# Kernel optimization log

Hardware: AMD Instinct MI355X
Metric: run time of the kernel (lower is better)

Reference implementation:

```python
import jax, jax.numpy as jnp
import numpy as np

L, D, H, FF = 4, 256, 8, 1024
B, S = 4, 1024
HD = D // H
EPS = 1e-5


def layer_norm(x, g, b):
    mu = jnp.mean(x, axis=-1, keepdims=True)
    var = jnp.mean(jnp.square(x - mu), axis=-1, keepdims=True)
    return (x - mu) * jax.lax.rsqrt(var + EPS) * g + b


def setup_inputs() -> dict:
    key = jax.random.key(0)
    ks = jax.random.split(key, 16)
    sd = 0.02
    return {
        "x": jax.random.normal(ks[0], (B, S, D), dtype=jnp.float32),
        "mask": jnp.ones((B, S), dtype=jnp.int32),
        # per-layer stacked params (leading dim L); Linear stored as (in, out)
        "qkv_w": jax.random.normal(ks[1], (L, D, 3 * D), dtype=jnp.float32) * sd,
        "qkv_b": jnp.zeros((L, 3 * D), dtype=jnp.float32),
        "fc_w": jax.random.normal(ks[2], (L, D, D), dtype=jnp.float32) * sd,
        "fc_b": jnp.zeros((L, D), dtype=jnp.float32),
        "ln1_g": jnp.ones((L, D), dtype=jnp.float32),
        "ln1_b": jnp.zeros((L, D), dtype=jnp.float32),
        "ln2_g": jnp.ones((L, D), dtype=jnp.float32),
        "ln2_b": jnp.zeros((L, D), dtype=jnp.float32),
        "ff1_w": jax.random.normal(ks[3], (L, D, FF), dtype=jnp.float32) * sd,
        "ff1_b": jnp.zeros((L, FF), dtype=jnp.float32),
        "ff2_w": jax.random.normal(ks[4], (L, FF, D), dtype=jnp.float32) * sd,
        "ff2_b": jnp.zeros((L, D), dtype=jnp.float32),
    }


def reference(x, mask, qkv_w, qkv_b, fc_w, fc_b, ln1_g, ln1_b, ln2_g, ln2_b,
              ff1_w, ff1_b, ff2_w, ff2_b):
    # mask: 1 = valid token, 0 = pad
    neg_inf = jnp.finfo(x.dtype).min
    key_mask = (mask == 0)[:, None, None, :]  # [B,1,1,S]
    for l in range(L):
        residual = x
        qkv = x @ qkv_w[l] + qkv_b[l]                       # [B,S,3D]
        q, k, v = jnp.split(qkv, 3, axis=-1)
        q = q.reshape(B, S, H, HD).transpose(0, 2, 1, 3)    # [B,H,S,hd]
        k = k.reshape(B, S, H, HD).transpose(0, 2, 1, 3)
        v = v.reshape(B, S, H, HD).transpose(0, 2, 1, 3)
        attn = jnp.einsum('bhqd,bhkd->bhqk', q, k)          # scale=1 (scale=False)
        attn = jnp.where(key_mask, neg_inf, attn)
        attn = jax.nn.softmax(attn, axis=-1)
        o = jnp.einsum('bhqk,bhkd->bhqd', attn, v)
        o = o.transpose(0, 2, 1, 3).reshape(B, S, D)
        o = o @ fc_w[l] + fc_b[l]
        x = layer_norm(o + residual, ln1_g[l], ln1_b[l])    # after_norm=True
        residual = x
        h = jax.nn.relu(x @ ff1_w[l] + ff1_b[l])
        h = h @ ff2_w[l] + ff2_b[l]
        x = layer_norm(residual + h, ln2_g[l], ln2_b[l])
    return x
```

## Files before the change

### kernel.cpp

```cpp
#include <hip/hip_runtime.h>
#include <hip/hip_bf16.h>
#include <math.h>

#define NL 4
#define DMODEL 256
#define NH 8
#define FFDIM 1024
#define BB 4
#define SS 1024
#define HDIM 32
#define MROWS (BB * SS)
#define LN_EPS 1e-5f

typedef __bf16 bf16x8 __attribute__((ext_vector_type(8)));
typedef float f32x4 __attribute__((ext_vector_type(4)));
typedef short s16x4 __attribute__((ext_vector_type(4)));
typedef unsigned int u32;

__device__ __forceinline__ ushort f2bf(float f) {
    uint u = __builtin_bit_cast(uint, f);
    u += 0x7fff + ((u >> 16) & 1);
    return (ushort)(u >> 16);
}
__device__ __forceinline__ uint pack2(float a, float b) {
    return (uint)f2bf(a) | ((uint)f2bf(b) << 16);
}

__device__ __forceinline__ int xcd_swz(int bid, int nwg) {
    return (bid & 7) * (nwg >> 3) + (bid >> 3);
}

template<int N> __device__ __forceinline__ void vmcnt_wait() {
    asm volatile("s_waitcnt vmcnt(%0)" :: "n"(N) : "memory");
}
__device__ __forceinline__ void raw_barrier() {
    asm volatile("s_barrier" ::: "memory");
}
__device__ __forceinline__ void lgkm0() {
    asm volatile("s_waitcnt lgkmcnt(0)" ::: "memory");
}

__device__ __forceinline__ void async_ld16(const void* g, void* l) {
    __builtin_amdgcn_global_load_lds(
        (const __attribute__((address_space(1))) u32*)g,
        (__attribute__((address_space(3))) u32*)l, 16, 0, 0);
}

#if __has_builtin(__builtin_amdgcn_ds_read_tr16_b64)
#define TR_BUILTIN 1
#else
#define TR_BUILTIN 0
#endif

__device__ __forceinline__ s16x4 tr16(const ushort* p) {
    __attribute__((address_space(3))) s16x4* ap =
        (__attribute__((address_space(3))) s16x4*)p;
#if TR_BUILTIN
    return __builtin_amdgcn_ds_read_tr16_b64(ap);
#else
    s16x4 r;
    asm volatile("ds_read_b64_tr_b16 %0, %1" : "=v"(r) : "v"(ap) : "memory");
    return r;
#endif
}
__device__ __forceinline__ void tr_fence() {
#if !TR_BUILTIN
    asm volatile("s_waitcnt lgkmcnt(0)" ::: "memory");
    __builtin_amdgcn_sched_barrier(0);
#endif
}

__global__ __launch_bounds__(256)
void wconv_all(const float* __restrict__ qkv_w, const float* __restrict__ fc_w,
               const float* __restrict__ ff1_w, const float* __restrict__ ff2_w,
               ushort* __restrict__ wq, ushort* __restrict__ wfc,
               ushort* __restrict__ wf1, ushort* __restrict__ wf2)
{
    const int l = blockIdx.z;
    int t = blockIdx.x;
    const float* src; ushort* dst; int K, N, nx;
    if (t < 192)      {          src = qkv_w; dst = wq;  K = 256;  N = 768;  nx = 24; }
    else if (t < 256) { t -= 192; src = fc_w;  dst = wfc; K = 256;  N = 256;  nx = 8; }
    else if (t < 512) { t -= 256; src = ff1_w; dst = wf1; K = 256;  N = 1024; nx = 32; }
    else              { t -= 512; src = ff2_w; dst = wf2; K = 1024; N = 256;  nx = 8; }
    src += (size_t)l * K * N;
    dst += (size_t)l * K * N;
    const int n0 = (t % nx) * 32, k0 = (t / nx) * 32;

    __shared__ ushort tt[32][33];
    const int tn = threadIdx.x & 31, tk8 = threadIdx.x >> 5;
    #pragma unroll
    for (int i = 0; i < 4; ++i)
        tt[tn][tk8 + i * 8] = f2bf(src[(size_t)(k0 + tk8 + i * 8) * N + n0 + tn]);
    __syncthreads();
    #pragma unroll
    for (int i = 0; i < 4; ++i)
        dst[(size_t)(n0 + tk8 + i * 8) * K + k0 + tn] = tt[tk8 + i * 8][tn];
}

__global__ __launch_bounds__(256)
void convert_x(const float* __restrict__ xin, float* __restrict__ x,
               ushort* __restrict__ xb)
{
    const size_t i = ((size_t)blockIdx.x * 256 + threadIdx.x) * 4;
    const float4 v = *reinterpret_cast<const float4*>(xin + i);
    *reinterpret_cast<float4*>(x + i) = v;
    uint2 p = make_uint2(pack2(v.x, v.y), pack2(v.z, v.w));
    *reinterpret_cast<uint2*>(xb + i) = p;
}

template<int BM, int BN, int WM, int WN, int ACT, int OBF>
__global__ __launch_bounds__(256)
void gemm_mfma(const ushort* __restrict__ A, const ushort* __restrict__ WT,
               const float* __restrict__ bias, float* __restrict__ Cf,
               ushort* __restrict__ Cb, int N, int K)
{
    constexpr int BK = 64;
    constexpr int WR = BM / WM;
    constexpr int WC = BN / WN;
    constexpr int MR = WR / 16, NR = WC / 16;
    constexpr int LSTG = BM / 32 + BN / 32;
    __shared__ __align__(16) ushort As[2][BM * BK];
    __shared__ __align__(16) ushort Bs[2][BN * BK];

    const int tid = threadIdx.x;
    const int lin = blockIdx.y * gridDim.x + blockIdx.x;
    const int work = xcd_swz(lin, gridDim.x * gridDim.y);
    const int m0 = (work / gridDim.x) * BM, n0 = (work % gridDim.x) * BN;
    const int wid = tid >> 6, lane = tid & 63;
    const int g = lane >> 4, c = lane & 15;
    const int wr = wid / WN, wc = wid % WN;

    auto stage = [&](int buf, int k0) {
        #pragma unroll
        for (int it = 0; it < (BM * BK * 2) / 4096; ++it) {
            const int o = tid * 16 + it * 4096;
            const int r = o >> 7;
            const int cb = (o & 127) ^ ((r & 7) << 4);
            async_ld16(A + (size_t)(m0 + r) * K + k0 + (cb >> 1),
                       (char*)&As[buf][0] + o);
        }
        #pragma unroll
        for (int it = 0; it < (BN * BK * 2) / 4096; ++it) {
            const int o = tid * 16 + it * 4096;
            const int r = o >> 7;
            const int cb = (o & 127) ^ ((r & 7) << 4);
            async_ld16(WT + (size_t)(n0 + r) * K + k0 + (cb >> 1),
                       (char*)&Bs[buf][0] + o);
        }
    };

    f32x4 acc[MR][NR] = {};

    stage(0, 0);

    int cur = 0;
    for (int k0 = 0; k0 < K; k0 += BK, cur ^= 1) {
        if (k0 + BK < K) { stage(cur ^ 1, k0 + BK); vmcnt_wait<LSTG>(); }
        else             { vmcnt_wait<0>(); }
        raw_barrier();

        #pragma unroll
        for (int ks = 0; ks < 2; ++ks) {
            bf16x8 af[MR], bfr[NR];
            #pragma unroll
            for (int mi = 0; mi < MR; ++mi) {
                const int row = wr * WR + mi * 16 + c;
                af[mi] = *(const bf16x8*)((const char*)&As[cur][0]
                    + row * 128 + ((ks * 64 + g * 16) ^ ((row & 7) << 4)));
            }
            #pragma unroll
            for (int ni = 0; ni < NR; ++ni) {
                const int row = wc * WC + ni * 16 + c;
                bfr[ni] = *(const bf16x8*)((const char*)&Bs[cur][0]
                    + row * 128 + ((ks * 64 + g * 16) ^ ((row & 7) << 4)));
            }
            #pragma unroll
            for (int mi = 0; mi < MR; ++mi)
                #pragma unroll
                for (int ni = 0; ni < NR; ++ni)
                    acc[mi][ni] = __builtin_amdgcn_mfma_f32_16x16x32_bf16(
                        af[mi], bfr[ni], acc[mi][ni], 0, 0, 0);
        }
        raw_barrier();
    }

    float bv[NR];
    #pragma unroll
    for (int ni = 0; ni < NR; ++ni)
        bv[ni] = bias[n0 + wc * WC + ni * 16 + c];

    #pragma unroll
    for (int mi = 0; mi < MR; ++mi) {
        #pragma unroll
        for (int j = 0; j < 4; ++j) {
            const int row = m0 + wr * WR + mi * 16 + g * 4 + j;
            #pragma unroll
            for (int ni = 0; ni < NR; ++ni) {
                float v = acc[mi][ni][j] + bv[ni];
                if (ACT) v = fmaxf(v, 0.f);
                const int col = n0 + wc * WC + ni * 16 + c;
                if (OBF) Cb[(size_t)row * N + col] = f2bf(v);
                else     Cf[(size_t)row * N + col] = v;
            }
        }
    }
}

__global__ __launch_bounds__(256)
void mlp_fused(const ushort* __restrict__ Aattn, const ushort* __restrict__ Wfc,
               const float* __restrict__ bfc, const float* __restrict__ g1,
               const float* __restrict__ be1, const ushort* __restrict__ W1,
               const float* __restrict__ b1, const ushort* __restrict__ W2,
               const float* __restrict__ b2, const float* __restrict__ g2,
               const float* __restrict__ be2, float* __restrict__ x,
               ushort* __restrict__ xb)
{
    __shared__ __align__(16) ushort As[2][16 * 64];
    __shared__ __align__(16) ushort Bs[2][256 * 64];
    __shared__ __align__(16) ushort ybf[16 * 256];
    __shared__ __align__(16) ushort hbuf[16 * 1024];
    __shared__ float rsum[4][16], rsq[4][16], mval[16], ival[16];

    const int tid = threadIdx.x;
    const int m0 = blockIdx.x * 16;
    const int wid = tid >> 6, lane = tid & 63;
    const int g = lane >> 4, c = lane & 15;

    auto stageB = [&](int buf, const ushort* src, int ldk) {
        #pragma unroll
        for (int it = 0; it < 8; ++it) {
            const int o = tid * 16 + it * 4096;
            const int r = o >> 7;
            const int cb = (o & 127) ^ ((r & 7) << 4);
            async_ld16(src + (size_t)r * ldk + (cb >> 1), (char*)&Bs[buf][0] + o);
        }
    };
    auto stageA = [&](int buf, int k0) {
        if (tid < 128) {
            const int o = tid * 16;
            const int r = o >> 7;
            const int cb = (o & 127) ^ ((r & 7) << 4);
            async_ld16(Aattn + (size_t)(m0 + r) * 256 + k0 + (cb >> 1),
                       (char*)&As[buf][0] + o);
        }
    };

    f32x4 acc[4] = {};
    const f32x4 zf = {0.f, 0.f, 0.f, 0.f};

    stageA(0, 0); stageB(0, Wfc, 256);
    int cur = 0;
    #pragma unroll
    for (int k = 0; k < 4; ++k, cur ^= 1) {
        if (k < 3) {
            stageA(cur ^ 1, (k + 1) * 64);
            stageB(cur ^ 1, Wfc + (k + 1) * 64, 256);
            if (tid < 128) vmcnt_wait<9>(); else vmcnt_wait<8>();
        } else {
            stageB(cur ^ 1, W1, 256);
            vmcnt_wait<8>();
        }
        raw_barrier();
        #pragma unroll
        for (int ks = 0; ks < 2; ++ks) {
            const bf16x8 af = *(const bf16x8*)((const char*)&As[cur][0]
                + c * 128 + ((ks * 64 + g * 16) ^ ((c & 7) << 4)));
            #pragma unroll
            for (int ni = 0; ni < 4; ++ni) {
                const int row = wid * 64 + ni * 16 + c;
                const bf16x8 bf = *(const bf16x8*)((const char*)&Bs[cur][0]
                    + row * 128 + ((ks * 64 + g * 16) ^ ((row & 7) << 4)));
                acc[ni] = __builtin_amdgcn_mfma_f32_16x16x32_bf16(af, bf, acc[ni], 0, 0, 0);
            }
        }
        raw_barrier();
    }

    float res[4][4];
    {
        float bv[4], gl[4], bl[4];
        #pragma unroll
        for (int ni = 0; ni < 4; ++ni) {
            const int col = wid * 64 + ni * 16 + c;
            bv[ni] = bfc[col]; gl[ni] = g1[col]; bl[ni] = be1[col];
        }
        #pragma unroll
        for (int j = 0; j < 4; ++j) {
            const int row = g * 4 + j;
            float s = 0.f;
            #pragma unroll
            for (int ni = 0; ni < 4; ++ni) {
                const int col = wid * 64 + ni * 16 + c;
                float vv = acc[ni][j] + bv[ni] + x[(size_t)(m0 + row) * 256 + col];
                acc[ni][j] = vv;
                s += vv;
            }
            #pragma unroll
            for (int off = 1; off < 16; off <<= 1) s += __shfl_xor(s, off);
            if (c == 0) rsum[wid][row] = s;
        }
        __syncthreads();
        if (tid < 16)
            mval[tid] = (rsum[0][tid] + rsum[1][tid] + rsum[2][tid] + rsum[3][tid])
                        * (1.f / 256);
        __syncthreads();
        #pragma unroll
        for (int j = 0; j < 4; ++j) {
            const int row = g * 4 + j;
            const float mean = mval[row];
            float q = 0.f;
            #pragma unroll
            for (int ni = 0; ni < 4; ++ni) {
                const float d = acc[ni][j] - mean;
                q += d * d;
            }
            #pragma unroll
            for (int off = 1; off < 16; off <<= 1) q += __shfl_xor(q, off);
            if (c == 0) rsq[wid][row] = q;
        }
        __syncthreads();
        if (tid < 16) {
            const float q = rsq[0][tid] + rsq[1][tid] + rsq[2][tid] + rsq[3][tid];
            ival[tid] = rsqrtf(q * (1.f / 256) + LN_EPS);
        }
        __syncthreads();
        #pragma unroll
        for (int j = 0; j < 4; ++j) {
            const int row = g * 4 + j;
            const float mean = mval[row], inv = ival[row];
            #pragma unroll
            for (int ni = 0; ni < 4; ++ni) {
                const int col = wid * 64 + ni * 16 + c;
                const float y = (acc[ni][j] - mean) * inv * gl[ni] + bl[ni];
                res[ni][j] = y;
                const int byteo = row * 512 + ((col * 2) ^ ((row & 7) << 4));
                *(ushort*)((char*)ybf + byteo) = f2bf(y);
                acc[ni][j] = 0.f;
            }
        }
    }
    lgkm0();
    raw_barrier();

    #pragma unroll 1
    for (int s = 0; s < 16; ++s, cur ^= 1) {
        const int kk = s & 3;
        if (s < 15) {
            const int s2 = s + 1;
            stageB(cur ^ 1, W1 + (size_t)((s2 >> 2) * 256) * 256 + (s2 & 3) * 64, 256);
            vmcnt_wait<8>();
        } else {
            stageB(cur ^ 1, W2, 1024);
            vmcnt_wait<8>();
        }
        raw_barrier();
        #pragma unroll
        for (int ks = 0; ks < 2; ++ks) {
            const int kbyte = (kk * 64 + ks * 32 + g * 8) * 2;
            const bf16x8 af = *(const bf16x8*)((const char*)ybf
                + c * 512 + (kbyte ^ ((c & 7) << 4)));
            #pragma unroll
            for (int ni = 0; ni < 4; ++ni) {
                const int row = wid * 64 + ni * 16 + c;
                const bf16x8 bf = *(const bf16x8*)((const char*)&Bs[cur][0]
                    + row * 128 + ((ks * 64 + g * 16) ^ ((row & 7) << 4)));
                acc[ni] = __builtin_amdgcn_mfma_f32_16x16x32_bf16(af, bf, acc[ni], 0, 0, 0);
            }
        }
        raw_barrier();
        if (kk == 3) {
            const int nt = s >> 2;
            #pragma unroll
            for (int j = 0; j < 4; ++j) {
                const int row = g * 4 + j;
                #pragma unroll
                for (int ni = 0; ni < 4; ++ni) {
                    const int col = nt * 256 + wid * 64 + ni * 16 + c;
                    const float h = fmaxf(acc[ni][j] + b1[col], 0.f);
                    const int byteo = row * 2048 + ((col * 2) ^ ((row & 7) << 4));
                    *(ushort*)((char*)hbuf + byteo) = f2bf(h);
                    acc[ni][j] = 0.f;
                }
            }
        }
    }
    lgkm0();
    raw_barrier();

    #pragma unroll 1
    for (int s = 0; s < 16; ++s, cur ^= 1) {
        if (s < 15) { stageB(cur ^ 1, W2 + (s + 1) * 64, 1024); vmcnt_wait<8>(); }
        else        { vmcnt_wait<0>(); }
        raw_barrier();
        #pragma unroll
        for (int ks = 0; ks < 2; ++ks) {
            const int kbyte = (s * 64 + ks * 32 + g * 8) * 2;
            const bf16x8 af = *(const bf16x8*)((const char*)hbuf
                + c * 2048 + (kbyte ^ ((c & 7) << 4)));
            #pragma unroll
            for (int ni = 0; ni < 4; ++ni) {
                const int row = wid * 64 + ni * 16 + c;
                const bf16x8 bf = *(const bf16x8*)((const char*)&Bs[cur][0]
                    + row * 128 + ((ks * 64 + g * 16) ^ ((row & 7) << 4)));
                acc[ni] = __builtin_amdgcn_mfma_f32_16x16x32_bf16(af, bf, acc[ni], 0, 0, 0);
            }
        }
        raw_barrier();
    }

    {
        float bv[4], gl[4], bl[4];
        #pragma unroll
        for (int ni = 0; ni < 4; ++ni) {
            const int col = wid * 64 + ni * 16 + c;
            bv[ni] = b2[col]; gl[ni] = g2[col]; bl[ni] = be2[col];
        }
        #pragma unroll
        for (int j = 0; j < 4; ++j) {
            const int row = g * 4 + j;
            float s = 0.f;
            #pragma unroll
            for (int ni = 0; ni < 4; ++ni) {
                float vv = acc[ni][j] + bv[ni] + res[ni][j];
                acc[ni][j] = vv;
                s += vv;
            }
            #pragma unroll
            for (int off = 1; off < 16; off <<= 1) s += __shfl_xor(s, off);
            if (c == 0) rsum[wid][row] = s;
        }
        __syncthreads();
        if (tid < 16)
            mval[tid] = (rsum[0][tid] + rsum[1][tid] + rsum[2][tid] + rsum[3][tid])
                        * (1.f / 256);
        __syncthreads();
        #pragma unroll
        for (int j = 0; j < 4; ++j) {
            const int row = g * 4 + j;
            const float mean = mval[row];
            float q = 0.f;
            #pragma unroll
            for (int ni = 0; ni < 4; ++ni) {
                const float d = acc[ni][j] - mean;
                q += d * d;
            }
            #pragma unroll
            for (int off = 1; off < 16; off <<= 1) q += __shfl_xor(q, off);
            if (c == 0) rsq[wid][row] = q;
        }
        __syncthreads();
        if (tid < 16) {
            const float q = rsq[0][tid] + rsq[1][tid] + rsq[2][tid] + rsq[3][tid];
            ival[tid] = rsqrtf(q * (1.f / 256) + LN_EPS);
        }
        __syncthreads();
        #pragma unroll
        for (int j = 0; j < 4; ++j) {
            const int row = g * 4 + j;
            const float mean = mval[row], inv = ival[row];
            #pragma unroll
            for (int ni = 0; ni < 4; ++ni) {
                const int col = wid * 64 + ni * 16 + c;
                const float y = (acc[ni][j] - mean) * inv * gl[ni] + bl[ni];
                x[(size_t)(m0 + row) * 256 + col] = y;
                xb[(size_t)(m0 + row) * 256 + col] = f2bf(y);
            }
        }
    }
}

__global__ __launch_bounds__(512)
void attn_mfma8(const ushort* __restrict__ qkv, const int* __restrict__ mask,
                ushort* __restrict__ out)
{
    const int tid = threadIdx.x;
    const int lane = tid & 63, wid = tid >> 6;
    const int g = lane >> 4, c = lane & 15;
    const int work = xcd_swz(blockIdx.x, 256);
    const int qblk = work & 7;
    const int bh = work >> 3;
    const int h = bh & (NH - 1), b = bh >> 3;
    const int q0 = qblk * 128 + wid * 16;

    __shared__ __align__(16) ushort Kb[2][128 * 32];
    __shared__ __align__(16) ushort Vs[2][2][128][16];
    __shared__ __align__(16) ushort Pl[8][16][136];
    __shared__ __align__(16) float  sbias[SS];
    __shared__ int mflag[8];

    const ushort* base  = qkv + (size_t)b * SS * 768;
    const ushort* kbase = base + DMODEL + h * HDIM;
    const ushort* vbase = base + 2 * DMODEL + h * HDIM;

    {
        const int i = tid * 2;
        const int2 mv = *reinterpret_cast<const int2*>(mask + b * SS + i);
        float2 bv;
        bv.x = mv.x ? 0.f : -3.4e38f;
        bv.y = mv.y ? 0.f : -3.4e38f;
        *reinterpret_cast<float2*>(&sbias[i]) = bv;
        const int miss = __any(!(mv.x && mv.y));
        if (lane == 0) mflag[wid] = miss;
    }

    const bf16x8 qfrag = *(const bf16x8*)(
        base + (size_t)(q0 + c) * 768 + h * HDIM + g * 8);

    const int o16   = tid * 16;
    const int krow  = o16 >> 6;
    const int kin   = (o16 & 63) ^ ((krow & 3) << 4);
    const int vhalf = o16 >> 12;
    const int vkey  = (o16 & 4095) >> 5;
    const int vd    = vhalf * 16 + (((o16 >> 4) & 1) << 3);

    #define STAGE(buf, koff)                                                   \
        do {                                                                   \
            async_ld16(kbase + (size_t)((koff) + krow) * 768 + (kin >> 1),     \
                       (char*)&Kb[buf][0] + o16);                              \
            async_ld16(vbase + (size_t)((koff) + vkey) * 768 + vd,             \
                       (char*)&Vs[buf][0][0][0] + o16);                        \
        } while (0)

    STAGE(0, 0);
    lgkm0();
    raw_barrier();
    const int anyMasked = mflag[0] | mflag[1] | mflag[2] | mflag[3]
                        | mflag[4] | mflag[5] | mflag[6] | mflag[7];

    float m = -1e30f, lpart = 0.f;
    f32x4 o0 = {0.f, 0.f, 0.f, 0.f}, o1 = {0.f, 0.f, 0.f, 0.f};
    const f32x4 zf = {0.f, 0.f, 0.f, 0.f};

    for (int t = 0; t < 8; ++t) {
        const int cur = t & 1;
        if (t < 7) { STAGE(cur ^ 1, (t + 1) * 128); vmcnt_wait<2>(); }
        else       { vmcnt_wait<0>(); }
        raw_barrier();

        f32x4 s[8];
        __builtin_amdgcn_s_setprio(1);
        #pragma unroll
        for (int kt = 0; kt < 8; ++kt) {
            const int row = kt * 16 + c;
            const bf16x8 kf = *(const bf16x8*)((const char*)&Kb[cur][0]
                + row * 64 + ((g * 16) ^ ((c & 3) << 4)));
            s[kt] = __builtin_amdgcn_mfma_f32_16x16x32_bf16(kf, qfrag, zf, 0, 0, 0);
        }
        __builtin_amdgcn_s_setprio(0);

        if (anyMasked) {
            #pragma unroll
            for (int kt = 0; kt < 8; ++kt) {
                const f32x4 bv = *reinterpret_cast<const f32x4*>(
                    &sbias[t * 128 + kt * 16 + g * 4]);
                #pragma unroll
                for (int r = 0; r < 4; ++r) s[kt][r] += bv[r];
            }
        }

        union UU { s16x4 h[2]; bf16x8 v; };
        UU u0[4], u1[4];
        #pragma unroll
        for (int ks = 0; ks < 4; ++ks) {
            const int vr0 = ks * 32 + g * 8;
            u0[ks].h[0] = tr16(&Vs[cur][0][vr0][c]);
            u0[ks].h[1] = tr16(&Vs[cur][0][vr0 + 4][c]);
            u1[ks].h[0] = tr16(&Vs[cur][1][vr0][c]);
            u1[ks].h[1] = tr16(&Vs[cur][1][vr0 + 4][c]);
        }

        float mx = fmaxf(fmaxf(s[0][0], s[0][1]), fmaxf(s[0][2], s[0][3]));
        #pragma unroll
        for (int kt = 1; kt < 8; ++kt)
            mx = fmaxf(mx, fmaxf(fmaxf(s[kt][0], s[kt][1]),
                                 fmaxf(s[kt][2], s[kt][3])));
        if (!__all(mx <= m + 8.f)) {
            float fm = fmaxf(mx, __shfl_xor(mx, 16));
            fm = fmaxf(fm, __shfl_xor(fm, 32));
            const float mn = fmaxf(m, fm);
            const float sc = __expf(m - mn);
            m = mn;
            lpart *= sc;
            float scr[4];
            #pragma unroll
            for (int r = 0; r < 4; ++r) scr[r] = __shfl(sc, g * 4 + r);
            #pragma unroll
            for (int r = 0; r < 4; ++r) { o0[r] *= scr[r]; o1[r] *= scr[r]; }
        }

        float ls = 0.f;
        #pragma unroll
        for (int kt = 0; kt < 8; ++kt) {
            const float p0 = __expf(s[kt][0] - m);
            const float p1 = __expf(s[kt][1] - m);
            const float p2 = __expf(s[kt][2] - m);
            const float p3 = __expf(s[kt][3] - m);
            ls += (p0 + p1) + (p2 + p3);
            uint2 pk2 = make_uint2(pack2(p0, p1), pack2(p2, p3));
            *reinterpret_cast<uint2*>(&Pl[wid][c][kt * 16 + g * 4]) = pk2;
        }
        lpart += ls;

        tr_fence();
        __builtin_amdgcn_s_setprio(1);
        #pragma unroll
        for (int ks = 0; ks < 4; ++ks) {
            const bf16x8 pa = *(const bf16x8*)&Pl[wid][c][ks * 32 + g * 8];
            o0 = __builtin_amdgcn_mfma_f32_16x16x32_bf16(pa, u0[ks].v, o0, 0, 0, 0);
            o1 = __builtin_amdgcn_mfma_f32_16x16x32_bf16(pa, u1[ks].v, o1, 0, 0, 0);
        }
        __builtin_amdgcn_s_setprio(0);
        raw_barrier();
    }
    #undef STAGE

    float lsum = lpart;
    lsum += __shfl_xor(lsum, 16);
    lsum += __shfl_xor(lsum, 32);
    const float rs = 1.f / lsum;
    float inv[4];
    #pragma unroll
    for (int r = 0; r < 4; ++r) inv[r] = __shfl(rs, g * 4 + r);
    #pragma unroll
    for (int r = 0; r < 4; ++r) {
        ushort* op = out + (size_t)(b * SS + q0 + g * 4 + r) * DMODEL + h * HDIM;
        op[c]      = f2bf(o0[r] * inv[r]);
        op[16 + c] = f2bf(o1[r] * inv[r]);
    }
}

extern "C" void kernel_launch(void* const* d_in, const int* in_sizes, int n_in,
                              void* d_out, int out_size, void* d_ws, size_t ws_size,
                              hipStream_t stream)
{
    const float* x_in   = (const float*)d_in[0];
    const int*   maskp  = (const int*)d_in[1];
    const float* qkv_w  = (const float*)d_in[2];
    const float* qkv_b  = (const float*)d_in[3];
    const float* fc_w   = (const float*)d_in[4];
    const float* fc_b   = (const float*)d_in[5];
    const float* ln1_g  = (const float*)d_in[6];
    const float* ln1_b  = (const float*)d_in[7];
    const float* ln2_g  = (const float*)d_in[8];
    const float* ln2_b  = (const float*)d_in[9];
    const float* ff1_w  = (const float*)d_in[10];
    const float* ff1_b  = (const float*)d_in[11];
    const float* ff2_w  = (const float*)d_in[12];
    const float* ff2_b  = (const float*)d_in[13];

    float* x = (float*)d_out;

    ushort* wt_qkv = (ushort*)d_ws;
    ushort* wt_fc  = wt_qkv + (size_t)NL * 768 * 256;
    ushort* wt_ff1 = wt_fc  + (size_t)NL * 256 * 256;
    ushort* wt_ff2 = wt_ff1 + (size_t)NL * 1024 * 256;
    ushort* big    = wt_ff2 + (size_t)NL * 256 * 1024;
    ushort* attn_bf= big + (size_t)MROWS * FFDIM;
    ushort* x_bf   = attn_bf + (size_t)MROWS * DMODEL;

    wconv_all<<<dim3(768, 1, NL), 256, 0, stream>>>(
        qkv_w, fc_w, ff1_w, ff2_w, wt_qkv, wt_fc, wt_ff1, wt_ff2);
    convert_x<<<dim3(MROWS * DMODEL / 1024), 256, 0, stream>>>(x_in, x, x_bf);

    for (int l = 0; l < NL; ++l) {
        gemm_mfma<64, 64, 2, 2, 0, 1><<<dim3(12, 64), 256, 0, stream>>>(
            x_bf, wt_qkv + (size_t)l * 768 * 256, qkv_b + l * 768,
            nullptr, big, 768, 256);
        attn_mfma8<<<dim3(256), 512, 0, stream>>>(big, maskp, attn_bf);
        mlp_fused<<<dim3(256), 256, 0, stream>>>(
            attn_bf, wt_fc + (size_t)l * 256 * 256, fc_b + l * 256,
            ln1_g + l * DMODEL, ln1_b + l * DMODEL,
            wt_ff1 + (size_t)l * 1024 * 256, ff1_b + l * FFDIM,
            wt_ff2 + (size_t)l * 256 * 1024, ff2_b + l * DMODEL,
            ln2_g + l * DMODEL, ln2_b + l * DMODEL, x, x_bf);
    }
}
```

Baseline: 222.5 us.

## Fuse next layer's QKV projection into the fused MLP kernel epilogue

The fused MLP kernel now keeps the final layer-norm output for its 16 rows in shared memory as bf16. It then runs the next layer's QKV GEMM directly over 12 double-buffered K-chunks of the QKV weights and writes the qkv buffer. This removes three separate QKV GEMM launches and the re-read of x_bf from global memory. In exchange, each MLP block does more serial work with only 256 blocks, which may lower GEMM efficiency compared with the separate 768-block tiled launch.

```diff
diff --git a/kernel.cpp b/kernel.cpp
--- a/kernel.cpp
+++ b/kernel.cpp
@@ -207,6 +207,7 @@
     }
 }
 
+template<int DO_QKV>
 __global__ __launch_bounds__(256)
 void mlp_fused(const ushort* __restrict__ Aattn, const ushort* __restrict__ Wfc,
                const float* __restrict__ bfc, const float* __restrict__ g1,
@@ -214,7 +215,8 @@
                const float* __restrict__ b1, const ushort* __restrict__ W2,
                const float* __restrict__ b2, const float* __restrict__ g2,
                const float* __restrict__ be2, float* __restrict__ x,
-               ushort* __restrict__ xb)
+               ushort* __restrict__ xb, const ushort* __restrict__ Wq,
+               const float* __restrict__ bq, ushort* __restrict__ qkvout)
 {
     __shared__ __align__(16) ushort As[2][16 * 64];
     __shared__ __align__(16) ushort Bs[2][256 * 64];
@@ -247,7 +249,6 @@
     };
 
     f32x4 acc[4] = {};
-    const f32x4 zf = {0.f, 0.f, 0.f, 0.f};
 
     stageA(0, 0); stageB(0, Wfc, 256);
     int cur = 0;
@@ -465,6 +466,57 @@
                 const float y = (acc[ni][j] - mean) * inv * gl[ni] + bl[ni];
                 x[(size_t)(m0 + row) * 256 + col] = y;
                 xb[(size_t)(m0 + row) * 256 + col] = f2bf(y);
+                if (DO_QKV) {
+                    const int byteo = row * 512 + ((col * 2) ^ ((row & 7) << 4));
+                    *(ushort*)((char*)ybf + byteo) = f2bf(y);
+                    acc[ni][j] = 0.f;
+                }
+            }
+        }
+    }
+
+    if (DO_QKV) {
+        lgkm0();
+        raw_barrier();
+        stageB(cur, Wq, 256);
+        #pragma unroll 1
+        for (int s = 0; s < 12; ++s, cur ^= 1) {
+            const int kk = s & 3;
+            if (s < 11) {
+                const int s2 = s + 1;
+                stageB(cur ^ 1, Wq + (size_t)((s2 >> 2) * 256) * 256 + (s2 & 3) * 64, 256);
+                vmcnt_wait<8>();
+            } else {
+                vmcnt_wait<0>();
+            }
+            raw_barrier();
+            #pragma unroll
+            for (int ks = 0; ks < 2; ++ks) {
+                const int kbyte = (kk * 64 + ks * 32 + g * 8) * 2;
+                const bf16x8 af = *(const bf16x8*)((const char*)ybf
+                    + c * 512 + (kbyte ^ ((c & 7) << 4)));
+                #pragma unroll
+                for (int ni = 0; ni < 4; ++ni) {
+                    const int row = wid * 64 + ni * 16 + c;
+                    const bf16x8 bf = *(const bf16x8*)((const char*)&Bs[cur][0]
+                        + row * 128 + ((ks * 64 + g * 16) ^ ((row & 7) << 4)));
+                    acc[ni] = __builtin_amdgcn_mfma_f32_16x16x32_bf16(af, bf, acc[ni], 0, 0, 0);
+                }
+            }
+            raw_barrier();
+            if (kk == 3) {
+                const int nt = s >> 2;
+                #pragma unroll
+                for (int j = 0; j < 4; ++j) {
+                    const int row = g * 4 + j;
+                    #pragma unroll
+                    for (int ni = 0; ni < 4; ++ni) {
+                        const int col = nt * 256 + wid * 64 + ni * 16 + c;
+                        const float v = acc[ni][j] + bq[col];
+                        qkvout[(size_t)(m0 + row) * 768 + col] = f2bf(v);
+                        acc[ni][j] = 0.f;
+                    }
+                }
             }
         }
     }
@@ -663,16 +715,27 @@
         qkv_w, fc_w, ff1_w, ff2_w, wt_qkv, wt_fc, wt_ff1, wt_ff2);
     convert_x<<<dim3(MROWS * DMODEL / 1024), 256, 0, stream>>>(x_in, x, x_bf);
 
+    gemm_mfma<64, 64, 2, 2, 0, 1><<<dim3(12, 64), 256, 0, stream>>>(
+        x_bf, wt_qkv, qkv_b, nullptr, big, 768, 256);
+
     for (int l = 0; l < NL; ++l) {
-        gemm_mfma<64, 64, 2, 2, 0, 1><<<dim3(12, 64), 256, 0, stream>>>(
-            x_bf, wt_qkv + (size_t)l * 768 * 256, qkv_b + l * 768,
-            nullptr, big, 768, 256);
         attn_mfma8<<<dim3(256), 512, 0, stream>>>(big, maskp, attn_bf);
-        mlp_fused<<<dim3(256), 256, 0, stream>>>(
-            attn_bf, wt_fc + (size_t)l * 256 * 256, fc_b + l * 256,
-            ln1_g + l * DMODEL, ln1_b + l * DMODEL,
-            wt_ff1 + (size_t)l * 1024 * 256, ff1_b + l * FFDIM,
-            wt_ff2 + (size_t)l * 256 * 1024, ff2_b + l * DMODEL,
-            ln2_g + l * DMODEL, ln2_b + l * DMODEL, x, x_bf);
-    }
-}
+        if (l < NL - 1) {
+            mlp_fused<1><<<dim3(256), 256, 0, stream>>>(
+                attn_bf, wt_fc + (size_t)l * 256 * 256, fc_b + l * 256,
+                ln1_g + l * DMODEL, ln1_b + l * DMODEL,
+                wt_ff1 + (size_t)l * 1024 * 256, ff1_b + l * FFDIM,
+                wt_ff2 + (size_t)l * 256 * 1024, ff2_b + l * DMODEL,
+                ln2_g + l * DMODEL, ln2_b + l * DMODEL, x, x_bf,
+                wt_qkv + (size_t)(l + 1) * 768 * 256, qkv_b + (l + 1) * 768, big);
+        } else {
+            mlp_fused<0><<<dim3(256), 256, 0, stream>>>(
+                attn_bf, wt_fc + (size_t)l * 256 * 256, fc_b + l * 256,
+                ln1_g + l * DMODEL, ln1_b + l * DMODEL,
+                wt_ff1 + (size_t)l * 1024 * 256, ff1_b + l * FFDIM,
+                wt_ff2 + (size_t)l * 256 * 1024, ff2_b + l * DMODEL,
+                ln2_g + l * DMODEL, ln2_b + l * DMODEL, x, x_bf,
+                nullptr, nullptr, nullptr);
+        }
+    }
+}
```

Measured after the change: 244.8 us. 1.1x slower.

## Warp-specialize mlp_fused into producer/consumer waves with triple-buffered weight staging

Applied to the files above, without the earlier changes.

Doubles the fused MLP block to 512 threads, where four waves issue only async global-to-LDS weight and activation loads and four waves do the MFMA math. The three separate GEMM phases (fc, ff1, ff2) are merged into one 36-step loop with a three-deep shared buffer and a two-step prefetch distance. The goal is to hide weight-load latency behind compute without the consumer waves stalling on the loads they issue. The cost is more LDS (a third buffer stage), extra barriers that the idle producer waves must also join during the layernorm phases, and possibly lower occupancy per CU.

```diff
diff --git a/kernel.cpp b/kernel.cpp
--- a/kernel.cpp
+++ b/kernel.cpp
@@ -207,7 +207,7 @@
     }
 }
 
-__global__ __launch_bounds__(256)
+__global__ __launch_bounds__(512)
 void mlp_fused(const ushort* __restrict__ Aattn, const ushort* __restrict__ Wfc,
                const float* __restrict__ bfc, const float* __restrict__ g1,
                const float* __restrict__ be1, const ushort* __restrict__ W1,
@@ -216,8 +216,8 @@
                const float* __restrict__ be2, float* __restrict__ x,
                ushort* __restrict__ xb)
 {
-    __shared__ __align__(16) ushort As[2][16 * 64];
-    __shared__ __align__(16) ushort Bs[2][256 * 64];
+    __shared__ __align__(16) ushort As3[3][16 * 64];
+    __shared__ __align__(16) ushort Bs3[3][256 * 64];
     __shared__ __align__(16) ushort ybf[16 * 256];
     __shared__ __align__(16) ushort hbuf[16 * 1024];
     __shared__ float rsum[4][16], rsq[4][16], mval[16], ival[16];
@@ -226,151 +226,162 @@
     const int m0 = blockIdx.x * 16;
     const int wid = tid >> 6, lane = tid & 63;
     const int g = lane >> 4, c = lane & 15;
-
-    auto stageB = [&](int buf, const ushort* src, int ldk) {
+    const bool consumer = (tid < 256);
+    const int ptid = tid - 256;
+    const int at = tid - 384;
+
+    auto stage_step = [&](int s, int b) {
+        const ushort* bsrc; int ldk;
+        if (s < 4)       { bsrc = Wfc + s * 64; ldk = 256; }
+        else if (s < 20) { const int t = s - 4;
+                           bsrc = W1 + (size_t)((t >> 2) * 256) * 256 + (t & 3) * 64;
+                           ldk = 256; }
+        else             { const int t = s - 20; bsrc = W2 + t * 64; ldk = 1024; }
         #pragma unroll
         for (int it = 0; it < 8; ++it) {
-            const int o = tid * 16 + it * 4096;
+            const int o = ptid * 16 + it * 4096;
             const int r = o >> 7;
             const int cb = (o & 127) ^ ((r & 7) << 4);
-            async_ld16(src + (size_t)r * ldk + (cb >> 1), (char*)&Bs[buf][0] + o);
-        }
-    };
-    auto stageA = [&](int buf, int k0) {
-        if (tid < 128) {
-            const int o = tid * 16;
+            async_ld16(bsrc + (size_t)r * ldk + (cb >> 1), (char*)&Bs3[b][0] + o);
+        }
+        if (s < 4 && at >= 0) {
+            const int o = at * 16;
             const int r = o >> 7;
             const int cb = (o & 127) ^ ((r & 7) << 4);
-            async_ld16(Aattn + (size_t)(m0 + r) * 256 + k0 + (cb >> 1),
-                       (char*)&As[buf][0] + o);
+            async_ld16(Aattn + (size_t)(m0 + r) * 256 + s * 64 + (cb >> 1),
+                       (char*)&As3[b][0] + o);
         }
     };
 
     f32x4 acc[4] = {};
-    const f32x4 zf = {0.f, 0.f, 0.f, 0.f};
-
-    stageA(0, 0); stageB(0, Wfc, 256);
-    int cur = 0;
-    #pragma unroll
-    for (int k = 0; k < 4; ++k, cur ^= 1) {
-        if (k < 3) {
-            stageA(cur ^ 1, (k + 1) * 64);
-            stageB(cur ^ 1, Wfc + (k + 1) * 64, 256);
-            if (tid < 128) vmcnt_wait<9>(); else vmcnt_wait<8>();
+    float res[4][4];
+
+    if (!consumer) {
+        stage_step(0, 0);
+        stage_step(1, 1);
+        if (wid >= 6) vmcnt_wait<9>(); else vmcnt_wait<8>();
+    }
+    raw_barrier();
+
+    #pragma unroll 1
+    for (int s = 0; s < 36; ++s) {
+        if (s == 4) {
+            if (consumer) {
+                float bv[4];
+                #pragma unroll
+                for (int ni = 0; ni < 4; ++ni)
+                    bv[ni] = bfc[wid * 64 + ni * 16 + c];
+                #pragma unroll
+                for (int j = 0; j < 4; ++j) {
+                    const int row = g * 4 + j;
+                    float sm = 0.f;
+                    #pragma unroll
+                    for (int ni = 0; ni < 4; ++ni) {
+                        const int col = wid * 64 + ni * 16 + c;
+                        float vv = acc[ni][j] + bv[ni]
+                                 + x[(size_t)(m0 + row) * 256 + col];
+                        acc[ni][j] = vv;
+                        sm += vv;
+                    }
+                    #pragma unroll
+                    for (int off = 1; off < 16; off <<= 1) sm += __shfl_xor(sm, off);
+                    if (c == 0) rsum[wid][row] = sm;
+                }
+            }
+            lgkm0(); raw_barrier();
+            if (consumer && tid < 16)
+                mval[tid] = (rsum[0][tid] + rsum[1][tid] + rsum[2][tid]
+                             + rsum[3][tid]) * (1.f / 256);
+            lgkm0(); raw_barrier();
+            if (consumer) {
+                #pragma unroll
+                for (int j = 0; j < 4; ++j) {
+                    const int row = g * 4 + j;
+                    const float mean = mval[row];
+                    float q = 0.f;
+                    #pragma unroll
+                    for (int ni = 0; ni < 4; ++ni) {
+                        const float d = acc[ni][j] - mean;
+                        q += d * d;
+                    }
+                    #pragma unroll
+                    for (int off = 1; off < 16; off <<= 1) q += __shfl_xor(q, off);
+                    if (c == 0) rsq[wid][row] = q;
+                }
+            }
+            lgkm0(); raw_barrier();
+            if (consumer && tid < 16) {
+                const float q = rsq[0][tid] + rsq[1][tid] + rsq[2][tid] + rsq[3][tid];
+                ival[tid] = rsqrtf(q * (1.f / 256) + LN_EPS);
+            }
+            lgkm0(); raw_barrier();
+            if (consumer) {
+                float gl[4], bl[4];
+                #pragma unroll
+                for (int ni = 0; ni < 4; ++ni) {
+                    const int col = wid * 64 + ni * 16 + c;
+                    gl[ni] = g1[col]; bl[ni] = be1[col];
+                }
+                #pragma unroll
+                for (int j = 0; j < 4; ++j) {
+                    const int row = g * 4 + j;
+                    const float mean = mval[row], inv = ival[row];
+                    #pragma unroll
+                    for (int ni = 0; ni < 4; ++ni) {
+                        const int col = wid * 64 + ni * 16 + c;
+                        const float y = (acc[ni][j] - mean) * inv * gl[ni] + bl[ni];
+                        res[ni][j] = y;
+                        const int byteo = row * 512 + ((col * 2) ^ ((row & 7) << 4));
+                        *(ushort*)((char*)ybf + byteo) = f2bf(y);
+                        acc[ni][j] = 0.f;
+                    }
+                }
+            }
+            lgkm0(); raw_barrier();
+        }
+        if (s == 20) { lgkm0(); raw_barrier(); }
+
+        if (consumer) {
+            const int b = s % 3;
+            #pragma unroll
+            for (int ks = 0; ks < 2; ++ks) {
+                bf16x8 af;
+                if (s < 4) {
+                    af = *(const bf16x8*)((const char*)&As3[b][0]
+                        + c * 128 + ((ks * 64 + g * 16) ^ ((c & 7) << 4)));
+                } else if (s < 20) {
+                    const int kk = (s - 4) & 3;
+                    const int kbyte = (kk * 64 + ks * 32 + g * 8) * 2;
+                    af = *(const bf16x8*)((const char*)ybf
+                        + c * 512 + (kbyte ^ ((c & 7) << 4)));
+                } else {
+                    const int t = s - 20;
+                    const int kbyte = (t * 64 + ks * 32 + g * 8) * 2;
+                    af = *(const bf16x8*)((const char*)hbuf
+                        + c * 2048 + (kbyte ^ ((c & 7) << 4)));
+                }
+                #pragma unroll
+                for (int ni = 0; ni < 4; ++ni) {
+                    const int row = wid * 64 + ni * 16 + c;
+                    const bf16x8 bf = *(const bf16x8*)((const char*)&Bs3[b][0]
+                        + row * 128 + ((ks * 64 + g * 16) ^ ((row & 7) << 4)));
+                    acc[ni] = __builtin_amdgcn_mfma_f32_16x16x32_bf16(
+                        af, bf, acc[ni], 0, 0, 0);
+                }
+            }
         } else {
-            stageB(cur ^ 1, W1, 256);
-            vmcnt_wait<8>();
+            if (s + 2 < 36) {
+                stage_step(s + 2, (s + 2) % 3);
+                if (s + 2 < 4 && wid >= 6) vmcnt_wait<9>();
+                else                       vmcnt_wait<8>();
+            } else {
+                vmcnt_wait<0>();
+            }
         }
         raw_barrier();
-        #pragma unroll
-        for (int ks = 0; ks < 2; ++ks) {
-            const bf16x8 af = *(const bf16x8*)((const char*)&As[cur][0]
-                + c * 128 + ((ks * 64 + g * 16) ^ ((c & 7) << 4)));
-            #pragma unroll
-            for (int ni = 0; ni < 4; ++ni) {
-                const int row = wid * 64 + ni * 16 + c;
-                const bf16x8 bf = *(const bf16x8*)((const char*)&Bs[cur][0]
-                    + row * 128 + ((ks * 64 + g * 16) ^ ((row & 7) << 4)));
-                acc[ni] = __builtin_amdgcn_mfma_f32_16x16x32_bf16(af, bf, acc[ni], 0, 0, 0);
-            }
-        }
-        raw_barrier();
-    }
-
-    float res[4][4];
-    {
-        float bv[4], gl[4], bl[4];
-        #pragma unroll
-        for (int ni = 0; ni < 4; ++ni) {
-            const int col = wid * 64 + ni * 16 + c;
-            bv[ni] = bfc[col]; gl[ni] = g1[col]; bl[ni] = be1[col];
-        }
-        #pragma unroll
-        for (int j = 0; j < 4; ++j) {
-            const int row = g * 4 + j;
-            float s = 0.f;
-            #pragma unroll
-            for (int ni = 0; ni < 4; ++ni) {
-                const int col = wid * 64 + ni * 16 + c;
-                float vv = acc[ni][j] + bv[ni] + x[(size_t)(m0 + row) * 256 + col];
-                acc[ni][j] = vv;
-                s += vv;
-            }
-            #pragma unroll
-            for (int off = 1; off < 16; off <<= 1) s += __shfl_xor(s, off);
-            if (c == 0) rsum[wid][row] = s;
-        }
-        __syncthreads();
-        if (tid < 16)
-            mval[tid] = (rsum[0][tid] + rsum[1][tid] + rsum[2][tid] + rsum[3][tid])
-                        * (1.f / 256);
-        __syncthreads();
-        #pragma unroll
-        for (int j = 0; j < 4; ++j) {
-            const int row = g * 4 + j;
-            const float mean = mval[row];
-            float q = 0.f;
-            #pragma unroll
-            for (int ni = 0; ni < 4; ++ni) {
-                const float d = acc[ni][j] - mean;
-                q += d * d;
-            }
-            #pragma unroll
-            for (int off = 1; off < 16; off <<= 1) q += __shfl_xor(q, off);
-            if (c == 0) rsq[wid][row] = q;
-        }
-        __syncthreads();
-        if (tid < 16) {
-            const float q = rsq[0][tid] + rsq[1][tid] + rsq[2][tid] + rsq[3][tid];
-            ival[tid] = rsqrtf(q * (1.f / 256) + LN_EPS);
-        }
-        __syncthreads();
-        #pragma unroll
-        for (int j = 0; j < 4; ++j) {
-            const int row = g * 4 + j;
-            const float mean = mval[row], inv = ival[row];
-            #pragma unroll
-            for (int ni = 0; ni < 4; ++ni) {
-                const int col = wid * 64 + ni * 16 + c;
-                const float y = (acc[ni][j] - mean) * inv * gl[ni] + bl[ni];
-                res[ni][j] = y;
-                const int byteo = row * 512 + ((col * 2) ^ ((row & 7) << 4));
-                *(ushort*)((char*)ybf + byteo) = f2bf(y);
-                acc[ni][j] = 0.f;
-            }
-        }
-    }
-    lgkm0();
-    raw_barrier();
-
-    #pragma unroll 1
-    for (int s = 0; s < 16; ++s, cur ^= 1) {
-        const int kk = s & 3;
-        if (s < 15) {
-            const int s2 = s + 1;
-            stageB(cur ^ 1, W1 + (size_t)((s2 >> 2) * 256) * 256 + (s2 & 3) * 64, 256);
-            vmcnt_wait<8>();
-        } else {
-            stageB(cur ^ 1, W2, 1024);
-            vmcnt_wait<8>();
-        }
-        raw_barrier();
-        #pragma unroll
-        for (int ks = 0; ks < 2; ++ks) {
-            const int kbyte = (kk * 64 + ks * 32 + g * 8) * 2;
-            const bf16x8 af = *(const bf16x8*)((const char*)ybf
-                + c * 512 + (kbyte ^ ((c & 7) << 4)));
-            #pragma unroll
-            for (int ni = 0; ni < 4; ++ni) {
-                const int row = wid * 64 + ni * 16 + c;
-                const bf16x8 bf = *(const bf16x8*)((const char*)&Bs[cur][0]
-                    + row * 128 + ((ks * 64 + g * 16) ^ ((row & 7) << 4)));
-                acc[ni] = __builtin_amdgcn_mfma_f32_16x16x32_bf16(af, bf, acc[ni], 0, 0, 0);
-            }
-        }
-        raw_barrier();
-        if (kk == 3) {
-            const int nt = s >> 2;
+
+        if (consumer && s >= 4 && s < 20 && ((s - 4) & 3) == 3) {
+            const int nt = (s - 4) >> 2;
             #pragma unroll
             for (int j = 0; j < 4; ++j) {
                 const int row = g * 4 + j;
@@ -385,56 +396,33 @@
             }
         }
     }
-    lgkm0();
-    raw_barrier();
-
-    #pragma unroll 1
-    for (int s = 0; s < 16; ++s, cur ^= 1) {
-        if (s < 15) { stageB(cur ^ 1, W2 + (s + 1) * 64, 1024); vmcnt_wait<8>(); }
-        else        { vmcnt_wait<0>(); }
-        raw_barrier();
-        #pragma unroll
-        for (int ks = 0; ks < 2; ++ks) {
-            const int kbyte = (s * 64 + ks * 32 + g * 8) * 2;
-            const bf16x8 af = *(const bf16x8*)((const char*)hbuf
-                + c * 2048 + (kbyte ^ ((c & 7) << 4)));
-            #pragma unroll
-            for (int ni = 0; ni < 4; ++ni) {
-                const int row = wid * 64 + ni * 16 + c;
-                const bf16x8 bf = *(const bf16x8*)((const char*)&Bs[cur][0]
-                    + row * 128 + ((ks * 64 + g * 16) ^ ((row & 7) << 4)));
-                acc[ni] = __builtin_amdgcn_mfma_f32_16x16x32_bf16(af, bf, acc[ni], 0, 0, 0);
-            }
-        }
-        raw_barrier();
-    }
-
-    {
-        float bv[4], gl[4], bl[4];
-        #pragma unroll
-        for (int ni = 0; ni < 4; ++ni) {
-            const int col = wid * 64 + ni * 16 + c;
-            bv[ni] = b2[col]; gl[ni] = g2[col]; bl[ni] = be2[col];
-        }
+
+    if (consumer) {
+        float bv[4];
+        #pragma unroll
+        for (int ni = 0; ni < 4; ++ni)
+            bv[ni] = b2[wid * 64 + ni * 16 + c];
         #pragma unroll
         for (int j = 0; j < 4; ++j) {
             const int row = g * 4 + j;
-            float s = 0.f;
+            float sm = 0.f;
             #pragma unroll
             for (int ni = 0; ni < 4; ++ni) {
                 float vv = acc[ni][j] + bv[ni] + res[ni][j];
                 acc[ni][j] = vv;
-                s += vv;
-            }
-            #pragma unroll
-            for (int off = 1; off < 16; off <<= 1) s += __shfl_xor(s, off);
-            if (c == 0) rsum[wid][row] = s;
-        }
-        __syncthreads();
-        if (tid < 16)
-            mval[tid] = (rsum[0][tid] + rsum[1][tid] + rsum[2][tid] + rsum[3][tid])
-                        * (1.f / 256);
-        __syncthreads();
+                sm += vv;
+            }
+            #pragma unroll
+            for (int off = 1; off < 16; off <<= 1) sm += __shfl_xor(sm, off);
+            if (c == 0) rsum[wid][row] = sm;
+        }
+    }
+    lgkm0(); raw_barrier();
+    if (consumer && tid < 16)
+        mval[tid] = (rsum[0][tid] + rsum[1][tid] + rsum[2][tid] + rsum[3][tid])
+                    * (1.f / 256);
+    lgkm0(); raw_barrier();
+    if (consumer) {
         #pragma unroll
         for (int j = 0; j < 4; ++j) {
             const int row = g * 4 + j;
@@ -449,12 +437,20 @@
             for (int off = 1; off < 16; off <<= 1) q += __shfl_xor(q, off);
             if (c == 0) rsq[wid][row] = q;
         }
-        __syncthreads();
-        if (tid < 16) {
-            const float q = rsq[0][tid] + rsq[1][tid] + rsq[2][tid] + rsq[3][tid];
-            ival[tid] = rsqrtf(q * (1.f / 256) + LN_EPS);
-        }
-        __syncthreads();
+    }
+    lgkm0(); raw_barrier();
+    if (consumer && tid < 16) {
+        const float q = rsq[0][tid] + rsq[1][tid] + rsq[2][tid] + rsq[3][tid];
+        ival[tid] = rsqrtf(q * (1.f / 256) + LN_EPS);
+    }
+    lgkm0(); raw_barrier();
+    if (consumer) {
+        float gl[4], bl[4];
+        #pragma unroll
+        for (int ni = 0; ni < 4; ++ni) {
+            const int col = wid * 64 + ni * 16 + c;
+            gl[ni] = g2[col]; bl[ni] = be2[col];
+        }
         #pragma unroll
         for (int j = 0; j < 4; ++j) {
             const int row = g * 4 + j;
@@ -668,7 +664,7 @@
             x_bf, wt_qkv + (size_t)l * 768 * 256, qkv_b + l * 768,
             nullptr, big, 768, 256);
         attn_mfma8<<<dim3(256), 512, 0, stream>>>(big, maskp, attn_bf);
-        mlp_fused<<<dim3(256), 256, 0, stream>>>(
+        mlp_fused<<<dim3(256), 512, 0, stream>>>(
             attn_bf, wt_fc + (size_t)l * 256 * 256, fc_b + l * 256,
             ln1_g + l * DMODEL, ln1_b + l * DMODEL,
             wt_ff1 + (size_t)l * 1024 * 256, ff1_b + l * FFDIM,
```

New measurement: 230.2 us. 3.5% more time.

## Triple-buffer weight staging in fused MLP kernel with unified step schedule

Applied to the files above, without the earlier changes.

Replaces the double-buffered A/B shared-memory staging in the fused fc+LN+FFN kernel with a three-deep ring buffer driven by a single global step index across the fc, FF1 and FF2 phases. Loads are issued two steps ahead, which gives memory latency more time to hide behind MFMA work, and the prefetch carries across phase boundaries. It also swaps __syncthreads in the layernorm reductions for an LDS-count wait plus a raw barrier so outstanding global prefetches are not drained. The cost is an extra 32KB+ of shared memory per block, which may lower occupancy, and more intricate vmcnt bookkeeping.

```diff
diff --git a/kernel.cpp b/kernel.cpp
--- a/kernel.cpp
+++ b/kernel.cpp
@@ -216,8 +216,8 @@
                const float* __restrict__ be2, float* __restrict__ x,
                ushort* __restrict__ xb)
 {
-    __shared__ __align__(16) ushort As[2][16 * 64];
-    __shared__ __align__(16) ushort Bs[2][256 * 64];
+    __shared__ __align__(16) ushort As3[3][16 * 64];
+    __shared__ __align__(16) ushort Bs3[3][256 * 64];
     __shared__ __align__(16) ushort ybf[16 * 256];
     __shared__ __align__(16) ushort hbuf[16 * 1024];
     __shared__ float rsum[4][16], rsq[4][16], mval[16], ival[16];
@@ -227,57 +227,68 @@
     const int wid = tid >> 6, lane = tid & 63;
     const int g = lane >> 4, c = lane & 15;
 
-    auto stageB = [&](int buf, const ushort* src, int ldk) {
+    auto stage_step = [&](int s) {
+        const int b = s % 3;
+        const ushort* bsrc; int ldk;
+        if (s < 4)       { bsrc = Wfc + s * 64; ldk = 256; }
+        else if (s < 20) { const int t = s - 4;
+                           bsrc = W1 + (size_t)((t >> 2) * 256) * 256 + (t & 3) * 64;
+                           ldk = 256; }
+        else             { const int t = s - 20; bsrc = W2 + t * 64; ldk = 1024; }
         #pragma unroll
         for (int it = 0; it < 8; ++it) {
             const int o = tid * 16 + it * 4096;
             const int r = o >> 7;
             const int cb = (o & 127) ^ ((r & 7) << 4);
-            async_ld16(src + (size_t)r * ldk + (cb >> 1), (char*)&Bs[buf][0] + o);
-        }
-    };
-    auto stageA = [&](int buf, int k0) {
-        if (tid < 128) {
+            async_ld16(bsrc + (size_t)r * ldk + (cb >> 1), (char*)&Bs3[b][0] + o);
+        }
+        if (s < 4 && tid < 128) {
             const int o = tid * 16;
             const int r = o >> 7;
             const int cb = (o & 127) ^ ((r & 7) << 4);
-            async_ld16(Aattn + (size_t)(m0 + r) * 256 + k0 + (cb >> 1),
-                       (char*)&As[buf][0] + o);
+            async_ld16(Aattn + (size_t)(m0 + r) * 256 + s * 64 + (cb >> 1),
+                       (char*)&As3[b][0] + o);
         }
     };
 
-    f32x4 acc[4] = {};
-    const f32x4 zf = {0.f, 0.f, 0.f, 0.f};
-
-    stageA(0, 0); stageB(0, Wfc, 256);
-    int cur = 0;
-    #pragma unroll
-    for (int k = 0; k < 4; ++k, cur ^= 1) {
-        if (k < 3) {
-            stageA(cur ^ 1, (k + 1) * 64);
-            stageB(cur ^ 1, Wfc + (k + 1) * 64, 256);
-            if (tid < 128) vmcnt_wait<9>(); else vmcnt_wait<8>();
-        } else {
-            stageB(cur ^ 1, W1, 256);
-            vmcnt_wait<8>();
-        }
-        raw_barrier();
+    auto mfma_step = [&](int b, const bf16x8& af0, const bf16x8& af1, f32x4* acc) {
+        const bf16x8 afs[2] = { af0, af1 };
         #pragma unroll
         for (int ks = 0; ks < 2; ++ks) {
-            const bf16x8 af = *(const bf16x8*)((const char*)&As[cur][0]
-                + c * 128 + ((ks * 64 + g * 16) ^ ((c & 7) << 4)));
             #pragma unroll
             for (int ni = 0; ni < 4; ++ni) {
                 const int row = wid * 64 + ni * 16 + c;
-                const bf16x8 bf = *(const bf16x8*)((const char*)&Bs[cur][0]
+                const bf16x8 bf = *(const bf16x8*)((const char*)&Bs3[b][0]
                     + row * 128 + ((ks * 64 + g * 16) ^ ((row & 7) << 4)));
-                acc[ni] = __builtin_amdgcn_mfma_f32_16x16x32_bf16(af, bf, acc[ni], 0, 0, 0);
-            }
-        }
-        raw_barrier();
-    }
-
+                acc[ni] = __builtin_amdgcn_mfma_f32_16x16x32_bf16(
+                    afs[ks], bf, acc[ni], 0, 0, 0);
+            }
+        }
+    };
+
+    f32x4 acc[4] = {};
     float res[4][4];
+
+    stage_step(0);
+    stage_step(1);
+
+    #pragma unroll
+    for (int s = 0; s < 4; ++s) {
+        stage_step(s + 2);
+        if (s == 0)      { if (tid < 128) vmcnt_wait<18>(); else vmcnt_wait<16>(); }
+        else if (s == 1) { if (tid < 128) vmcnt_wait<18>(); else vmcnt_wait<16>(); }
+        else if (s == 2) { if (tid < 128) vmcnt_wait<17>(); else vmcnt_wait<16>(); }
+        else             { vmcnt_wait<16>(); }
+        raw_barrier();
+        const int b = s % 3;
+        const bf16x8 af0 = *(const bf16x8*)((const char*)&As3[b][0]
+            + c * 128 + ((0 * 64 + g * 16) ^ ((c & 7) << 4)));
+        const bf16x8 af1 = *(const bf16x8*)((const char*)&As3[b][0]
+            + c * 128 + ((1 * 64 + g * 16) ^ ((c & 7) << 4)));
+        mfma_step(b, af0, af1, acc);
+        raw_barrier();
+    }
+
     {
         float bv[4], gl[4], bl[4];
         #pragma unroll
@@ -300,11 +311,11 @@
             for (int off = 1; off < 16; off <<= 1) s += __shfl_xor(s, off);
             if (c == 0) rsum[wid][row] = s;
         }
-        __syncthreads();
+        lgkm0(); raw_barrier();
         if (tid < 16)
             mval[tid] = (rsum[0][tid] + rsum[1][tid] + rsum[2][tid] + rsum[3][tid])
                         * (1.f / 256);
-        __syncthreads();
+        lgkm0(); raw_barrier();
         #pragma unroll
         for (int j = 0; j < 4; ++j) {
             const int row = g * 4 + j;
@@ -319,12 +330,12 @@
             for (int off = 1; off < 16; off <<= 1) q += __shfl_xor(q, off);
             if (c == 0) rsq[wid][row] = q;
         }
-        __syncthreads();
+        lgkm0(); raw_barrier();
         if (tid < 16) {
             const float q = rsq[0][tid] + rsq[1][tid] + rsq[2][tid] + rsq[3][tid];
             ival[tid] = rsqrtf(q * (1.f / 256) + LN_EPS);
         }
-        __syncthreads();
+        lgkm0(); raw_barrier();
         #pragma unroll
         for (int j = 0; j < 4; ++j) {
             const int row = g * 4 + j;
@@ -344,33 +355,20 @@
     raw_barrier();
 
     #pragma unroll 1
-    for (int s = 0; s < 16; ++s, cur ^= 1) {
-        const int kk = s & 3;
-        if (s < 15) {
-            const int s2 = s + 1;
-            stageB(cur ^ 1, W1 + (size_t)((s2 >> 2) * 256) * 256 + (s2 & 3) * 64, 256);
-            vmcnt_wait<8>();
-        } else {
-            stageB(cur ^ 1, W2, 1024);
-            vmcnt_wait<8>();
-        }
-        raw_barrier();
-        #pragma unroll
-        for (int ks = 0; ks < 2; ++ks) {
-            const int kbyte = (kk * 64 + ks * 32 + g * 8) * 2;
-            const bf16x8 af = *(const bf16x8*)((const char*)ybf
-                + c * 512 + (kbyte ^ ((c & 7) << 4)));
-            #pragma unroll
-            for (int ni = 0; ni < 4; ++ni) {
-                const int row = wid * 64 + ni * 16 + c;
-                const bf16x8 bf = *(const bf16x8*)((const char*)&Bs[cur][0]
-                    + row * 128 + ((ks * 64 + g * 16) ^ ((row & 7) << 4)));
-                acc[ni] = __builtin_amdgcn_mfma_f32_16x16x32_bf16(af, bf, acc[ni], 0, 0, 0);
-            }
-        }
+    for (int s = 4; s < 20; ++s) {
+        stage_step(s + 2);
+        vmcnt_wait<16>();
+        raw_barrier();
+        const int b = s % 3;
+        const int kk = (s - 4) & 3;
+        const bf16x8 af0 = *(const bf16x8*)((const char*)ybf
+            + c * 512 + (((kk * 64 + 0 * 32 + g * 8) * 2) ^ ((c & 7) << 4)));
+        const bf16x8 af1 = *(const bf16x8*)((const char*)ybf
+            + c * 512 + (((kk * 64 + 1 * 32 + g * 8) * 2) ^ ((c & 7) << 4)));
+        mfma_step(b, af0, af1, acc);
         raw_barrier();
         if (kk == 3) {
-            const int nt = s >> 2;
+            const int nt = (s - 4) >> 2;
             #pragma unroll
             for (int j = 0; j < 4; ++j) {
                 const int row = g * 4 + j;
@@ -389,23 +387,18 @@
     raw_barrier();
 
     #pragma unroll 1
-    for (int s = 0; s < 16; ++s, cur ^= 1) {
-        if (s < 15) { stageB(cur ^ 1, W2 + (s + 1) * 64, 1024); vmcnt_wait<8>(); }
-        else        { vmcnt_wait<0>(); }
-        raw_barrier();
-        #pragma unroll
-        for (int ks = 0; ks < 2; ++ks) {
-            const int kbyte = (s * 64 + ks * 32 + g * 8) * 2;
-            const bf16x8 af = *(const bf16x8*)((const char*)hbuf
-                + c * 2048 + (kbyte ^ ((c & 7) << 4)));
-            #pragma unroll
-            for (int ni = 0; ni < 4; ++ni) {
-                const int row = wid * 64 + ni * 16 + c;
-                const bf16x8 bf = *(const bf16x8*)((const char*)&Bs[cur][0]
-                    + row * 128 + ((ks * 64 + g * 16) ^ ((row & 7) << 4)));
-                acc[ni] = __builtin_amdgcn_mfma_f32_16x16x32_bf16(af, bf, acc[ni], 0, 0, 0);
-            }
-        }
+    for (int s = 20; s < 36; ++s) {
+        if (s + 2 < 36) { stage_step(s + 2); vmcnt_wait<16>(); }
+        else if (s == 34) vmcnt_wait<8>();
+        else              vmcnt_wait<0>();
+        raw_barrier();
+        const int b = s % 3;
+        const int t = s - 20;
+        const bf16x8 af0 = *(const bf16x8*)((const char*)hbuf
+            + c * 2048 + (((t * 64 + 0 * 32 + g * 8) * 2) ^ ((c & 7) << 4)));
+        const bf16x8 af1 = *(const bf16x8*)((const char*)hbuf
+            + c * 2048 + (((t * 64 + 1 * 32 + g * 8) * 2) ^ ((c & 7) << 4)));
+        mfma_step(b, af0, af1, acc);
         raw_barrier();
     }
 
@@ -430,11 +423,11 @@
             for (int off = 1; off < 16; off <<= 1) s += __shfl_xor(s, off);
             if (c == 0) rsum[wid][row] = s;
         }
-        __syncthreads();
+        lgkm0(); raw_barrier();
         if (tid < 16)
             mval[tid] = (rsum[0][tid] + rsum[1][tid] + rsum[2][tid] + rsum[3][tid])
                         * (1.f / 256);
-        __syncthreads();
+        lgkm0(); raw_barrier();
         #pragma unroll
         for (int j = 0; j < 4; ++j) {
             const int row = g * 4 + j;
@@ -449,12 +442,12 @@
             for (int off = 1; off < 16; off <<= 1) q += __shfl_xor(q, off);
             if (c == 0) rsq[wid][row] = q;
         }
-        __syncthreads();
+        lgkm0(); raw_barrier();
         if (tid < 16) {
             const float q = rsq[0][tid] + rsq[1][tid] + rsq[2][tid] + rsq[3][tid];
             ival[tid] = rsqrtf(q * (1.f / 256) + LN_EPS);
         }
-        __syncthreads();
+        lgkm0(); raw_barrier();
         #pragma unroll
         for (int j = 0; j < 4; ++j) {
             const int row = g * 4 + j;
```

Result: slower. 245.0 us (+10.1%).
